# Performance work log

Hardware: AMD Instinct MI355X
Metric: run time of the kernel (lower is better)

Reference implementation:

```python
import jax, jax.numpy as jnp
import numpy as np

D_MODEL = 1024
NUM_HEADS = 16
HEAD_DIM = D_MODEL // NUM_HEADS
THETA = 10000.0


def _init_linear(key, d_out, d_in):
    sigma = np.sqrt(2.0 / (d_in + d_out))
    w = jax.random.truncated_normal(key, -3.0, 3.0, (d_out, d_in), dtype=jnp.float32)
    return w * sigma


def setup_inputs() -> dict:
    key = jax.random.key(0)
    kh, kq, kk, kv, ko = jax.random.split(key, 5)
    h = jax.random.normal(kh, (2, 2048, D_MODEL), dtype=jnp.float32)
    return {
        "h": h,
        "wq": _init_linear(kq, D_MODEL, D_MODEL),
        "wk": _init_linear(kk, D_MODEL, D_MODEL),
        "wv": _init_linear(kv, D_MODEL, D_MODEL),
        "wo": _init_linear(ko, D_MODEL, D_MODEL),
    }


def _rope(x, pos):
    # x: [B, H, T, dh]; rotate interleaved pairs (..., 2k, 2k+1)
    dh = x.shape[-1]
    freq = THETA ** (-jnp.arange(0, dh // 2, dtype=jnp.float32) / (dh // 2))
    ang = pos[:, None] * freq[None, :]            # [T, dh/2]
    cos, sin = jnp.cos(ang), jnp.sin(ang)
    xr = x.reshape(*x.shape[:-1], dh // 2, 2)
    x0, x1 = xr[..., 0], xr[..., 1]
    out = jnp.stack((cos * x0 - sin * x1, sin * x0 + cos * x1), axis=-1)
    return out.reshape(x.shape)


def reference(h, wq, wk, wv, wo):
    B, T, D = h.shape
    Hn, dh = NUM_HEADS, HEAD_DIM

    def split_heads(x):  # [B,T,D] -> [B,H,T,dh]
        return x.reshape(B, T, Hn, dh).transpose(0, 2, 1, 3)

    Q = split_heads(h @ wq.T)
    K = split_heads(h @ wk.T)
    V = split_heads(h @ wv.T)

    pos = jnp.arange(T, dtype=jnp.float32)
    Q = _rope(Q, pos)
    K = _rope(K, pos)

    scores = jnp.einsum('bhqd,bhkd->bhqk', Q, K) / jnp.sqrt(jnp.float32(dh))
    mask = jnp.tril(jnp.ones((T, T), dtype=bool))
    scores = jnp.where(mask, scores, -jnp.inf)
    attn = jax.nn.softmax(scores, axis=-1)
    out = jnp.einsum('bhqk,bhkd->bhqd', attn, V)   # [B,H,T,dh]
    out = out.transpose(0, 2, 1, 3).reshape(B, T, D)
    return out @ wo.T
```

## Files before the change

kernel.cpp:

```cpp
#include <hip/hip_runtime.h>
#include <math.h>

typedef __bf16 bf16_t;
typedef __bf16 v8bf __attribute__((ext_vector_type(8)));
typedef __bf16 v4bf __attribute__((ext_vector_type(4)));
typedef float  v4f  __attribute__((ext_vector_type(4)));

#define AS1 __attribute__((address_space(1)))
#define AS3 __attribute__((address_space(3)))

static __device__ __forceinline__ void load_lds16(const bf16_t* g, bf16_t* l) {
    __builtin_amdgcn_global_load_lds((AS1 void*)const_cast<bf16_t*>(g),
                                     (AS3 void*)l, 16, 0, 0);
}

static __device__ __forceinline__ void fast_sincos(float ang, float* sn, float* cs) {
    float rv = ang * 0.15915494309189535f;
    rv -= floorf(rv);
    const float a = rv * 6.283185307179586f;
    *sn = __sinf(a);
    *cs = __cosf(a);
}

__global__ __launch_bounds__(256) void cvt_fp32_bf16(
    const float* __restrict__ h,  const float* __restrict__ wq,
    const float* __restrict__ wk, const float* __restrict__ wv,
    const float* __restrict__ wo,
    bf16_t* __restrict__ hb,  bf16_t* __restrict__ wqb,
    bf16_t* __restrict__ wkb, bf16_t* __restrict__ wvb,
    bf16_t* __restrict__ wob)
{
    const size_t HM = (size_t)4 << 20;
    const size_t i8 = ((size_t)blockIdx.x * 256 + threadIdx.x) * 8;
    const float* src; bf16_t* dst; size_t off;
    if (i8 < HM) { src = h; dst = hb; off = i8; }
    else {
        const size_t r = (i8 - HM) >> 20;
        off = (i8 - HM) & (((size_t)1 << 20) - 1);
        src = (r == 0) ? wq  : (r == 1) ? wk  : (r == 2) ? wv  : wo;
        dst = (r == 0) ? wqb : (r == 1) ? wkb : (r == 2) ? wvb : wob;
    }
    const float4 a = *(const float4*)(src + off);
    const float4 b = *(const float4*)(src + off + 4);
    v8bf o;
    o[0]=(bf16_t)a.x; o[1]=(bf16_t)a.y; o[2]=(bf16_t)a.z; o[3]=(bf16_t)a.w;
    o[4]=(bf16_t)b.x; o[5]=(bf16_t)b.y; o[6]=(bf16_t)b.z; o[7]=(bf16_t)b.w;
    *(v8bf*)(dst + off) = o;
}

__global__ __launch_bounds__(256) void qkv_gemm_rope(
    const bf16_t* __restrict__ A,
    const bf16_t* __restrict__ wq,
    const bf16_t* __restrict__ wk,
    const bf16_t* __restrict__ wv,
    bf16_t* __restrict__ qo, bf16_t* __restrict__ ko, bf16_t* __restrict__ vo)
{
    __shared__ __align__(16) bf16_t smem[17408];
    bf16_t* As = smem;
    bf16_t* Bs = smem + 4096;

    const int tid = threadIdx.x;
    const int n0  = blockIdx.x * 128;
    const int m0  = blockIdx.y * 128;
    const int sel = n0 >> 10;
    const bf16_t* W = (sel == 0) ? wq : (sel == 1) ? wk : wv;
    const int wr0 = n0 & 1023;

    const int wave = tid >> 6;
    const int lane = tid & 63;
    const int l16  = lane & 15;
    const int quad = lane >> 4;
    const int wrow = (wave >> 1) * 64;
    const int wcol = (wave & 1) * 64;

    v4f acc[4][4];
    #pragma unroll
    for (int i = 0; i < 4; ++i)
        #pragma unroll
        for (int j = 0; j < 4; ++j) acc[i][j] = (v4f)(0.0f);

    for (int kt = 0; kt < 32; ++kt) {
        const int k0 = kt * 32;
        #pragma unroll
        for (int rep = 0; rep < 2; ++rep) {
            const int c   = rep * 256 + tid;
            const int row = c >> 2;
            const int col = (c & 3) * 8;
            load_lds16(A + (size_t)(m0 + row) * 1024 + k0 + col, &As[c * 8]);
            load_lds16(W + (size_t)(wr0 + row) * 1024 + k0 + col, &Bs[c * 8]);
        }
        __syncthreads();

        v8bf af[4], bfb[4];
        #pragma unroll
        for (int i = 0; i < 4; ++i) {
            af[i]  = *(const v8bf*)&As[(wrow + i * 16 + l16) * 32 + quad * 8];
            bfb[i] = *(const v8bf*)&Bs[(wcol + i * 16 + l16) * 32 + quad * 8];
        }
        #pragma unroll
        for (int i = 0; i < 4; ++i)
            #pragma unroll
            for (int j = 0; j < 4; ++j)
                acc[i][j] = __builtin_amdgcn_mfma_f32_16x16x32_bf16(
                    af[i], bfb[j], acc[i][j], 0, 0, 0);
        __syncthreads();
    }

    bf16_t* Ls = smem + wave * 4352;
    const int bq     = (m0 + wrow) >> 11;
    const int hd     = ((n0 + wcol) >> 6) & 15;
    const int t_base = (m0 + wrow) & 2047;

    if (sel < 2) {
        bf16_t* OUT = (sel == 0) ? qo : ko;
        #pragma unroll
        for (int i = 0; i < 4; ++i) {
            #pragma unroll
            for (int j = 0; j < 4; ++j) {
                #pragma unroll
                for (int r = 0; r < 4; ++r) {
                    const int mrow = i * 16 + quad * 4 + r;
                    const int dcol = j * 16 + l16;
                    float v = acc[i][j][r];
                    const float vp = __shfl_xor(v, 1);
                    const int t  = t_base + mrow;
                    const int kk = dcol >> 1;
                    const float freq = exp2f((float)kk * -0.4152410118609203f);
                    float sn, cs;
                    fast_sincos((float)t * freq, &sn, &cs);
                    v = ((dcol & 1) == 0) ? (cs * v - sn * vp) : (sn * vp + cs * v);
                    Ls[mrow * 68 + dcol] = (bf16_t)v;
                }
            }
        }
        #pragma unroll
        for (int s = 0; s < 8; ++s) {
            const int row = s * 8 + (lane >> 3);
            const int off = (lane & 7) * 8;
            const v8bf vv = *(const v8bf*)&Ls[row * 68 + off];
            *(v8bf*)(OUT + (((size_t)(bq * 16 + hd) * 2048) + t_base + row) * 64 + off) = vv;
        }
    } else {
        #pragma unroll
        for (int i = 0; i < 4; ++i)
            #pragma unroll
            for (int j = 0; j < 4; ++j) {
                v4bf p;
                #pragma unroll
                for (int r = 0; r < 4; ++r) p[r] = (bf16_t)acc[i][j][r];
                *(v4bf*)&Ls[(j * 16 + l16) * 68 + i * 16 + quad * 4] = p;
            }
        #pragma unroll
        for (int s = 0; s < 8; ++s) {
            const int drow = s * 8 + (lane >> 3);
            const int off  = (lane & 7) * 8;
            const v8bf vv = *(const v8bf*)&Ls[drow * 68 + off];
            *(v8bf*)(vo + (((size_t)(bq * 16 + hd) * 64) + drow) * 2048 + t_base + off) = vv;
        }
    }
}

__global__ __launch_bounds__(512, 4) void attn_mfma(
    const bf16_t* __restrict__ qg,
    const bf16_t* __restrict__ kg,
    const bf16_t* __restrict__ vtg,
    bf16_t* __restrict__ og)
{
    __shared__ __align__(16) bf16_t Ks[2][64 * 72];
    __shared__ __align__(16) bf16_t Vs[2][64 * 72];
    __shared__ __align__(16) bf16_t Ps[8][16 * 72];

    const int tid  = threadIdx.x;
    const int wave = tid >> 6;
    const int lane = tid & 63;
    const int l16  = lane & 15;
    const int quad = lane >> 4;

    const int i  = blockIdx.x;
    const int tt = i >> 3;
    const int u  = tt & 15;
    const int g  = tt >> 4;
    const int q128 = (((g + 1) >> 1) & 1) ? (15 - u) : u;
    const int bh = (i & 7) * 4 + g;
    const int b = bh >> 4, hh = bh & 15;

    const bf16_t* Kb = kg  + (size_t)bh * 2048 * 64;
    const bf16_t* Vb = vtg + (size_t)bh * 64 * 2048;

    const int qglb = q128 * 128 + wave * 16 + l16;
    const int diag_kt = 2 * q128 + (wave >> 2);
    const int ktmax = 2 * q128 + 1;

    const bf16_t* qrow = qg + ((size_t)bh * 2048 + qglb) * 64;
    v8bf qf[2];
    qf[0] = *(const v8bf*)(qrow + quad * 8);
    qf[1] = *(const v8bf*)(qrow + 32 + quad * 8);
    #pragma unroll
    for (int e = 0; e < 8; ++e) {
        qf[0][e] = (bf16_t)((float)qf[0][e] * 0.18033688011112042f);
        qf[1][e] = (bf16_t)((float)qf[1][e] * 0.18033688011112042f);
    }

    float m_r = -1e30f, l_r = 0.0f;
    v4f o_acc[4];
    #pragma unroll
    for (int d = 0; d < 4; ++d) o_acc[d] = (v4f)(0.0f);

    const int srow = tid >> 3;
    const int scol = (tid & 7) * 8;
    {
        const v8bf k0 = *(const v8bf*)(Kb + (size_t)srow * 64 + scol);
        const v8bf v0 = *(const v8bf*)(Vb + (size_t)srow * 2048 + scol);
        *(v8bf*)&Ks[0][srow * 72 + scol] = k0;
        *(v8bf*)&Vs[0][srow * 72 + scol] = v0;
    }

    for (int kt = 0; kt <= ktmax; ++kt) {
        const int cur = kt & 1;
        const int nxt = cur ^ 1;
        __syncthreads();

        v8bf kreg, vreg;
        if (kt < ktmax) {
            kreg = *(const v8bf*)(Kb + ((size_t)(kt + 1) * 64 + srow) * 64 + scol);
            vreg = *(const v8bf*)(Vb + (size_t)srow * 2048 + (kt + 1) * 64 + scol);
        }

        const bool active = (kt * 64) <= (q128 * 128 + wave * 16 + 15);
        if (active) {
            v4f s_acc[4];
            #pragma unroll
            for (int kblk = 0; kblk < 4; ++kblk) s_acc[kblk] = (v4f)(0.0f);
            #pragma unroll
            for (int kblk = 0; kblk < 4; ++kblk) {
                const v8bf kf0 = *(const v8bf*)&Ks[cur][(kblk * 16 + l16) * 72 + quad * 8];
                const v8bf kf1 = *(const v8bf*)&Ks[cur][(kblk * 16 + l16) * 72 + 32 + quad * 8];
                s_acc[kblk] = __builtin_amdgcn_mfma_f32_16x16x32_bf16(
                    kf0, qf[0], s_acc[kblk], 0, 0, 0);
                s_acc[kblk] = __builtin_amdgcn_mfma_f32_16x16x32_bf16(
                    kf1, qf[1], s_acc[kblk], 0, 0, 0);
            }

            if (kt == diag_kt) {
                #pragma unroll
                for (int kblk = 0; kblk < 4; ++kblk)
                    #pragma unroll
                    for (int r = 0; r < 4; ++r)
                        if (kt * 64 + kblk * 16 + quad * 4 + r > qglb)
                            s_acc[kblk][r] = -1e30f;
            }

            float mx = -1e30f;
            #pragma unroll
            for (int kblk = 0; kblk < 4; ++kblk)
                #pragma unroll
                for (int r = 0; r < 4; ++r) mx = fmaxf(mx, s_acc[kblk][r]);
            mx = fmaxf(mx, __shfl_xor(mx, 16));
            mx = fmaxf(mx, __shfl_xor(mx, 32));
            const float m_new = fmaxf(m_r, mx);
            float ssum = 0.0f;
            #pragma unroll
            for (int kblk = 0; kblk < 4; ++kblk)
                #pragma unroll
                for (int r = 0; r < 4; ++r) {
                    const float p = exp2f(s_acc[kblk][r] - m_new);
                    s_acc[kblk][r] = p;
                    ssum += p;
                }
            ssum += __shfl_xor(ssum, 16);
            ssum += __shfl_xor(ssum, 32);
            const float alpha = exp2f(m_r - m_new);
            l_r = l_r * alpha + ssum;
            m_r = m_new;

            #pragma unroll
            for (int kblk = 0; kblk < 4; ++kblk) {
                v4bf p;
                #pragma unroll
                for (int r = 0; r < 4; ++r) p[r] = (bf16_t)s_acc[kblk][r];
                *(v4bf*)&Ps[wave][l16 * 72 + kblk * 16 + quad * 4] = p;
            }
            #pragma unroll
            for (int d = 0; d < 4; ++d) o_acc[d] *= alpha;

            const v8bf pf0 = *(const v8bf*)&Ps[wave][l16 * 72 + quad * 8];
            const v8bf pf1 = *(const v8bf*)&Ps[wave][l16 * 72 + 32 + quad * 8];
            #pragma unroll
            for (int dblk = 0; dblk < 4; ++dblk) {
                const v8bf vf0 = *(const v8bf*)&Vs[cur][(dblk * 16 + l16) * 72 + quad * 8];
                const v8bf vf1 = *(const v8bf*)&Vs[cur][(dblk * 16 + l16) * 72 + 32 + quad * 8];
                o_acc[dblk] = __builtin_amdgcn_mfma_f32_16x16x32_bf16(
                    vf0, pf0, o_acc[dblk], 0, 0, 0);
                o_acc[dblk] = __builtin_amdgcn_mfma_f32_16x16x32_bf16(
                    vf1, pf1, o_acc[dblk], 0, 0, 0);
            }
        }

        if (kt < ktmax) {
            *(v8bf*)&Ks[nxt][srow * 72 + scol] = kreg;
            *(v8bf*)&Vs[nxt][srow * 72 + scol] = vreg;
        }
    }

    const float inv_l = 1.0f / l_r;
    const size_t base = ((size_t)b * 2048 + qglb) * 1024 + hh * 64;
    #pragma unroll
    for (int dblk = 0; dblk < 4; ++dblk) {
        v4bf o;
        #pragma unroll
        for (int r = 0; r < 4; ++r) o[r] = (bf16_t)(o_acc[dblk][r] * inv_l);
        *(v4bf*)(og + base + dblk * 16 + quad * 4) = o;
    }
}

__global__ __launch_bounds__(256) void out_gemm(
    const bf16_t* __restrict__ A,
    const bf16_t* __restrict__ W,
    float* __restrict__ C)
{
    __shared__ __align__(16) float smemf[4352];
    bf16_t* As = (bf16_t*)smemf;
    bf16_t* Bs = As + 4096;

    const int tid = threadIdx.x;
    const int n0  = blockIdx.x * 64;
    const int m0  = blockIdx.y * 128;

    const int wave = tid >> 6;
    const int lane = tid & 63;
    const int l16  = lane & 15;
    const int quad = lane >> 4;
    const int wrow = (wave >> 1) * 64;
    const int wcol = (wave & 1) * 32;

    v4f acc[4][2];
    #pragma unroll
    for (int i = 0; i < 4; ++i)
        #pragma unroll
        for (int j = 0; j < 2; ++j) acc[i][j] = (v4f)(0.0f);

    for (int kt = 0; kt < 32; ++kt) {
        const int k0 = kt * 32;
        #pragma unroll
        for (int rep = 0; rep < 2; ++rep) {
            const int c   = rep * 256 + tid;
            const int row = c >> 2;
            const int col = (c & 3) * 8;
            load_lds16(A + (size_t)(m0 + row) * 1024 + k0 + col, &As[c * 8]);
        }
        {
            const int row = tid >> 2;
            const int col = (tid & 3) * 8;
            load_lds16(W + (size_t)(n0 + row) * 1024 + k0 + col, &Bs[tid * 8]);
        }
        __syncthreads();

        v8bf af[4], bfb[2];
        #pragma unroll
        for (int i = 0; i < 4; ++i)
            af[i]  = *(const v8bf*)&As[(wrow + i * 16 + l16) * 32 + quad * 8];
        #pragma unroll
        for (int j = 0; j < 2; ++j)
            bfb[j] = *(const v8bf*)&Bs[(wcol + j * 16 + l16) * 32 + quad * 8];
        #pragma unroll
        for (int i = 0; i < 4; ++i)
            #pragma unroll
            for (int j = 0; j < 2; ++j)
                acc[i][j] = __builtin_amdgcn_mfma_f32_16x16x32_bf16(
                    af[i], bfb[j], acc[i][j], 0, 0, 0);
        __syncthreads();
    }

    float* Lw = smemf + wave * 1088;
    #pragma unroll
    for (int half = 0; half < 2; ++half) {
        #pragma unroll
        for (int ii = 0; ii < 2; ++ii) {
            const int i = half * 2 + ii;
            #pragma unroll
            for (int j = 0; j < 2; ++j)
                #pragma unroll
                for (int r = 0; r < 4; ++r)
                    Lw[(ii * 16 + quad * 4 + r) * 34 + j * 16 + l16] = acc[i][j][r];
        }
        #pragma unroll
        for (int s = 0; s < 8; ++s) {
            const int row = s * 4 + (lane >> 4);
            const float2 vv = *(const float2*)&Lw[row * 34 + l16 * 2];
            *(float2*)(C + (size_t)(m0 + wrow + half * 32 + row) * 1024
                         + n0 + wcol + l16 * 2) = vv;
        }
    }
}

extern "C" void kernel_launch(void* const* d_in, const int* in_sizes, int n_in,
                              void* d_out, int out_size, void* d_ws, size_t ws_size,
                              hipStream_t stream) {
    const float* h  = (const float*)d_in[0];
    const float* wq = (const float*)d_in[1];
    const float* wk = (const float*)d_in[2];
    const float* wv = (const float*)d_in[3];
    const float* wo = (const float*)d_in[4];

    const size_t NH = (size_t)4096 * 1024;
    const size_t NW = (size_t)1024 * 1024;

    bf16_t* hb  = (bf16_t*)d_ws;
    bf16_t* wqb = hb  + NH;
    bf16_t* wkb = wqb + NW;
    bf16_t* wvb = wkb + NW;
    bf16_t* wob = wvb + NW;
    bf16_t* qw  = wob + NW;
    bf16_t* kw  = qw + NH;
    bf16_t* vw  = kw + NH;
    bf16_t* og  = hb;

    cvt_fp32_bf16<<<dim3(4096), dim3(256), 0, stream>>>(
        h, wq, wk, wv, wo, hb, wqb, wkb, wvb, wob);
    qkv_gemm_rope<<<dim3(24, 32), dim3(256), 0, stream>>>(
        hb, wqb, wkb, wvb, qw, kw, vw);
    attn_mfma<<<dim3(512), dim3(512), 0, stream>>>(qw, kw, vw, og);
    out_gemm<<<dim3(16, 32), dim3(256), 0, stream>>>(og, wob, (float*)d_out);
}
```

Baseline: 187.4 us.

## Fuse fp32-to-bf16 conversion into QKV GEMM and compute softmax row sums via MFMA

The separate conversion pass over h, wq, wk and wv is removed. The QKV GEMM now loads fp32 tiles directly, converts them in registers and stores bf16 to LDS, instead of using async global-to-LDS loads. Only wo is still pre-converted. In attention, the per-row softmax sum is accumulated with an extra MFMA against a ones vector rather than scalar adds plus cross-lane shuffles. This trades a full extra memory pass for twice the global read bytes per GEMM tile (re-read across 24 column blocks) and synchronous loads that lose the async LDS path.

```diff
diff --git a/kernel.cpp b/kernel.cpp
--- a/kernel.cpp
+++ b/kernel.cpp
@@ -22,37 +22,23 @@
     *cs = __cosf(a);
 }
 
-__global__ __launch_bounds__(256) void cvt_fp32_bf16(
-    const float* __restrict__ h,  const float* __restrict__ wq,
-    const float* __restrict__ wk, const float* __restrict__ wv,
-    const float* __restrict__ wo,
-    bf16_t* __restrict__ hb,  bf16_t* __restrict__ wqb,
-    bf16_t* __restrict__ wkb, bf16_t* __restrict__ wvb,
-    bf16_t* __restrict__ wob)
+__global__ __launch_bounds__(256) void cvt_wo(
+    const float* __restrict__ wo, bf16_t* __restrict__ wob)
 {
-    const size_t HM = (size_t)4 << 20;
     const size_t i8 = ((size_t)blockIdx.x * 256 + threadIdx.x) * 8;
-    const float* src; bf16_t* dst; size_t off;
-    if (i8 < HM) { src = h; dst = hb; off = i8; }
-    else {
-        const size_t r = (i8 - HM) >> 20;
-        off = (i8 - HM) & (((size_t)1 << 20) - 1);
-        src = (r == 0) ? wq  : (r == 1) ? wk  : (r == 2) ? wv  : wo;
-        dst = (r == 0) ? wqb : (r == 1) ? wkb : (r == 2) ? wvb : wob;
-    }
-    const float4 a = *(const float4*)(src + off);
-    const float4 b = *(const float4*)(src + off + 4);
+    const float4 a = *(const float4*)(wo + i8);
+    const float4 b = *(const float4*)(wo + i8 + 4);
     v8bf o;
     o[0]=(bf16_t)a.x; o[1]=(bf16_t)a.y; o[2]=(bf16_t)a.z; o[3]=(bf16_t)a.w;
     o[4]=(bf16_t)b.x; o[5]=(bf16_t)b.y; o[6]=(bf16_t)b.z; o[7]=(bf16_t)b.w;
-    *(v8bf*)(dst + off) = o;
+    *(v8bf*)(wob + i8) = o;
 }
 
 __global__ __launch_bounds__(256) void qkv_gemm_rope(
-    const bf16_t* __restrict__ A,
-    const bf16_t* __restrict__ wq,
-    const bf16_t* __restrict__ wk,
-    const bf16_t* __restrict__ wv,
+    const float* __restrict__ A,
+    const float* __restrict__ wq,
+    const float* __restrict__ wk,
+    const float* __restrict__ wv,
     bf16_t* __restrict__ qo, bf16_t* __restrict__ ko, bf16_t* __restrict__ vo)
 {
     __shared__ __align__(16) bf16_t smem[17408];
@@ -63,7 +49,7 @@
     const int n0  = blockIdx.x * 128;
     const int m0  = blockIdx.y * 128;
     const int sel = n0 >> 10;
-    const bf16_t* W = (sel == 0) ? wq : (sel == 1) ? wk : wv;
+    const float* W = (sel == 0) ? wq : (sel == 1) ? wk : wv;
     const int wr0 = n0 & 1023;
 
     const int wave = tid >> 6;
@@ -86,8 +72,19 @@
             const int c   = rep * 256 + tid;
             const int row = c >> 2;
             const int col = (c & 3) * 8;
-            load_lds16(A + (size_t)(m0 + row) * 1024 + k0 + col, &As[c * 8]);
-            load_lds16(W + (size_t)(wr0 + row) * 1024 + k0 + col, &Bs[c * 8]);
+            const float* pa = A + (size_t)(m0 + row) * 1024 + k0 + col;
+            const float* pb = W + (size_t)(wr0 + row) * 1024 + k0 + col;
+            const float4 a0 = *(const float4*)pa;
+            const float4 a1 = *(const float4*)(pa + 4);
+            const float4 b0 = *(const float4*)pb;
+            const float4 b1 = *(const float4*)(pb + 4);
+            v8bf av, bv;
+            av[0] = (bf16_t)a0.x; av[1] = (bf16_t)a0.y; av[2] = (bf16_t)a0.z; av[3] = (bf16_t)a0.w;
+            av[4] = (bf16_t)a1.x; av[5] = (bf16_t)a1.y; av[6] = (bf16_t)a1.z; av[7] = (bf16_t)a1.w;
+            bv[0] = (bf16_t)b0.x; bv[1] = (bf16_t)b0.y; bv[2] = (bf16_t)b0.z; bv[3] = (bf16_t)b0.w;
+            bv[4] = (bf16_t)b1.x; bv[5] = (bf16_t)b1.y; bv[6] = (bf16_t)b1.z; bv[7] = (bf16_t)b1.w;
+            *(v8bf*)&As[c * 8] = av;
+            *(v8bf*)&Bs[c * 8] = bv;
         }
         __syncthreads();
 
@@ -201,7 +198,12 @@
         qf[1][e] = (bf16_t)((float)qf[1][e] * 0.18033688011112042f);
     }
 
-    float m_r = -1e30f, l_r = 0.0f;
+    v8bf ones1;
+    #pragma unroll
+    for (int e = 0; e < 8; ++e) ones1[e] = (bf16_t)1.0f;
+
+    float m_r = -1e30f;
+    v4f l_acc = (v4f)(0.0f);
     v4f o_acc[4];
     #pragma unroll
     for (int d = 0; d < 4; ++d) o_acc[d] = (v4f)(0.0f);
@@ -258,20 +260,13 @@
             mx = fmaxf(mx, __shfl_xor(mx, 16));
             mx = fmaxf(mx, __shfl_xor(mx, 32));
             const float m_new = fmaxf(m_r, mx);
-            float ssum = 0.0f;
+            const float alpha = exp2f(m_r - m_new);
+            m_r = m_new;
             #pragma unroll
             for (int kblk = 0; kblk < 4; ++kblk)
                 #pragma unroll
-                for (int r = 0; r < 4; ++r) {
-                    const float p = exp2f(s_acc[kblk][r] - m_new);
-                    s_acc[kblk][r] = p;
-                    ssum += p;
-                }
-            ssum += __shfl_xor(ssum, 16);
-            ssum += __shfl_xor(ssum, 32);
-            const float alpha = exp2f(m_r - m_new);
-            l_r = l_r * alpha + ssum;
-            m_r = m_new;
+                for (int r = 0; r < 4; ++r)
+                    s_acc[kblk][r] = exp2f(s_acc[kblk][r] - m_new);
 
             #pragma unroll
             for (int kblk = 0; kblk < 4; ++kblk) {
@@ -282,6 +277,7 @@
             }
             #pragma unroll
             for (int d = 0; d < 4; ++d) o_acc[d] *= alpha;
+            l_acc *= alpha;
 
             const v8bf pf0 = *(const v8bf*)&Ps[wave][l16 * 72 + quad * 8];
             const v8bf pf1 = *(const v8bf*)&Ps[wave][l16 * 72 + 32 + quad * 8];
@@ -294,6 +290,8 @@
                 o_acc[dblk] = __builtin_amdgcn_mfma_f32_16x16x32_bf16(
                     vf1, pf1, o_acc[dblk], 0, 0, 0);
             }
+            l_acc = __builtin_amdgcn_mfma_f32_16x16x32_bf16(ones1, pf0, l_acc, 0, 0, 0);
+            l_acc = __builtin_amdgcn_mfma_f32_16x16x32_bf16(ones1, pf1, l_acc, 0, 0, 0);
         }
 
         if (kt < ktmax) {
@@ -302,7 +300,7 @@
         }
     }
 
-    const float inv_l = 1.0f / l_r;
+    const float inv_l = 1.0f / l_acc[0];
     const size_t base = ((size_t)b * 2048 + qglb) * 1024 + hh * 64;
     #pragma unroll
     for (int dblk = 0; dblk < 4; ++dblk) {
@@ -405,20 +403,15 @@
     const size_t NH = (size_t)4096 * 1024;
     const size_t NW = (size_t)1024 * 1024;
 
-    bf16_t* hb  = (bf16_t*)d_ws;
-    bf16_t* wqb = hb  + NH;
-    bf16_t* wkb = wqb + NW;
-    bf16_t* wvb = wkb + NW;
-    bf16_t* wob = wvb + NW;
+    bf16_t* wob = (bf16_t*)d_ws;
     bf16_t* qw  = wob + NW;
     bf16_t* kw  = qw + NH;
     bf16_t* vw  = kw + NH;
-    bf16_t* og  = hb;
-
-    cvt_fp32_bf16<<<dim3(4096), dim3(256), 0, stream>>>(
-        h, wq, wk, wv, wo, hb, wqb, wkb, wvb, wob);
+    bf16_t* og  = vw + NH;
+
+    cvt_wo<<<dim3(512), dim3(256), 0, stream>>>(wo, wob);
     qkv_gemm_rope<<<dim3(24, 32), dim3(256), 0, stream>>>(
-        hb, wqb, wkb, wvb, qw, kw, vw);
+        h, wq, wk, wv, qw, kw, vw);
     attn_mfma<<<dim3(512), dim3(512), 0, stream>>>(qw, kw, vw, og);
     out_gemm<<<dim3(16, 32), dim3(256), 0, stream>>>(og, wob, (float*)d_out);
 }
```

After: 194.2 us. 3.6% more time.
